# Kernel tuning notes

Hardware: AMD Instinct MI355X
Metric: run time of the kernel (lower is better)

Reference implementation:

```python
import jax, jax.numpy as jnp
import numpy as np

HEADS = 8
LN_EPS = 1e-5


def _layernorm(x, g, b):
    mu = x.mean(-1, keepdims=True)
    var = jnp.var(x, axis=-1, keepdims=True)  # biased, matches torch LayerNorm
    return (x - mu) / jnp.sqrt(var + LN_EPS) * g + b


def setup_inputs() -> dict:
    key = jax.random.key(0)
    ks = jax.random.split(key, 5)
    Q, N, D = 4, 2048, 512  # [query-groups, tokens, model dim]
    return {
        "q": jax.random.normal(ks[0], (Q, N, D), jnp.float32),
        "k": jax.random.normal(ks[1], (Q, N, D), jnp.float32),
        "v": jax.random.normal(ks[2], (Q, N, D), jnp.float32),
        "ln_gamma": jnp.ones((D,), jnp.float32),
        "ln_beta": jnp.zeros((D,), jnp.float32),
        "w_in": jax.random.normal(ks[3], (D, D), jnp.float32) * 0.02,   # torch Linear weight [inner_dim, dim]
        "w_out": jax.random.normal(ks[4], (D, D), jnp.float32) * 0.02,  # [dim, inner_dim]
        "b_out": jnp.zeros((D,), jnp.float32),
        "cov_w_raw": jnp.float32(0.6),
        "var_w_raw": jnp.float32(0.2),
    }


def reference(q, k, v, ln_gamma, ln_beta, w_in, w_out, b_out, cov_w_raw, var_w_raw):
    H = HEADS

    def proj(t):
        x = _layernorm(t, ln_gamma, ln_beta) @ w_in.T  # [Q,N,inner]
        Qd, Nd, I = x.shape
        return x.reshape(Qd, Nd, H, I // H).transpose(2, 0, 1, 3)  # [H,Q,N,d]

    f_q, f_k, f_v = proj(q), proj(k), proj(v)
    d = f_q.shape[-1]

    # cosine similarity component
    dots = jnp.einsum('hqnd,hqmd->hqnm', f_q, f_k)
    qn = jnp.linalg.norm(f_q, axis=-1)  # [H,Q,N]
    kn = jnp.linalg.norm(f_k, axis=-1)
    cosine_sim = dots / (qn[..., :, None] * kn[..., None, :])

    # centered covariance component
    qc = f_q - f_q.mean(-1, keepdims=True)
    kc = f_k - f_k.mean(-1, keepdims=True)
    cov_component = jnp.einsum('hqnd,hqmd->hqnm', qc, kc) / d

    # variance product component (torch.var is unbiased -> ddof=1)
    q_var = jnp.var(f_q, axis=-1, ddof=1)  # [H,Q,N]
    k_var = jnp.var(f_k, axis=-1, ddof=1)
    var_component = q_var[..., :, None] * k_var[..., None, :] / d

    cov_w = jax.nn.sigmoid(cov_w_raw)
    var_w = jax.nn.sigmoid(var_w_raw)
    cos_w = 1.0 - cov_w - var_w
    attn = cos_w * cosine_sim + cov_w * cov_component + var_w * var_component

    out = jnp.einsum('hqnm,hqmd->hqnd', attn, f_v)
    out = out.transpose(1, 2, 0, 3).reshape(q.shape[0], q.shape[1], -1)  # q n (h d)
    return out @ w_out.T + b_out
```

## Files before the change

kernel.cpp:

```cpp
#include <hip/hip_runtime.h>
#include <hip/hip_bf16.h>
#include <math.h>

#define D_MODEL 512
#define NTOK 2048
#define QGRP 4
#define NHEAD 8
#define HDIM 64
#define ROWS_PER_T (QGRP * NTOK)
#define LN_EPS 1e-5f
#define NCHUNK 16

typedef __attribute__((ext_vector_type(8))) short short8;
typedef __attribute__((ext_vector_type(8))) __bf16 bf16x8;
typedef __attribute__((ext_vector_type(4))) float f32x4;

__device__ inline void split2(float y, ushort& h, ushort& l) {
    __hip_bfloat16 hb = __float2bfloat16(y);
    float hf = __bfloat162float(hb);
    __hip_bfloat16 lb = __float2bfloat16(y - hf);
    h = *reinterpret_cast<ushort*>(&hb);
    l = *reinterpret_cast<ushort*>(&lb);
}

__device__ inline float b2f(ushort u) {
    unsigned int x = ((unsigned int)u) << 16;
    return __uint_as_float(x);
}

__device__ inline void split8v(const float4& p0, const float4& p1, bf16x8& bh, bf16x8& bl) {
    float xv[8] = {p0.x, p0.y, p0.z, p0.w, p1.x, p1.y, p1.z, p1.w};
    ushort hs[8], ls[8];
#pragma unroll
    for (int j = 0; j < 8; ++j) split2(xv[j], hs[j], ls[j]);
    bh = *(const bf16x8*)hs;
    bl = *(const bf16x8*)ls;
}

__global__ __launch_bounds__(256)
void ln_split3_kernel(const float* __restrict__ q, const float* __restrict__ k,
                      const float* __restrict__ v, const float* __restrict__ gamma,
                      const float* __restrict__ beta,
                      ushort* __restrict__ A3h, ushort* __restrict__ A3l) {
    int wave = threadIdx.x >> 6, lane = threadIdx.x & 63;
    size_t row = (size_t)blockIdx.x * 4 + wave;
    int t = (int)(row >> 13);
    size_t r = row & 8191;
    const float* src = (t == 0 ? q : (t == 1 ? k : v)) + r * D_MODEL + lane * 8;
    float4 a = *(const float4*)src;
    float4 b = *(const float4*)(src + 4);
    float s  = a.x + a.y + a.z + a.w + b.x + b.y + b.z + b.w;
    float sq = a.x*a.x + a.y*a.y + a.z*a.z + a.w*a.w
             + b.x*b.x + b.y*b.y + b.z*b.z + b.w*b.w;
    for (int m = 1; m < 64; m <<= 1) {
        s  += __shfl_xor(s, m);
        sq += __shfl_xor(sq, m);
    }
    float mu   = s * (1.0f / (float)D_MODEL);
    float var  = sq * (1.0f / (float)D_MODEL) - mu * mu;
    float rstd = 1.0f / sqrtf(var + LN_EPS);
    float4 g0 = *(const float4*)(gamma + lane * 8);
    float4 g1 = *(const float4*)(gamma + lane * 8 + 4);
    float4 t0 = *(const float4*)(beta + lane * 8);
    float4 t1 = *(const float4*)(beta + lane * 8 + 4);
    float xv[8] = {a.x, a.y, a.z, a.w, b.x, b.y, b.z, b.w};
    float gv[8] = {g0.x, g0.y, g0.z, g0.w, g1.x, g1.y, g1.z, g1.w};
    float bv[8] = {t0.x, t0.y, t0.z, t0.w, t1.x, t1.y, t1.z, t1.w};
    ushort hs[8], ls[8];
#pragma unroll
    for (int j = 0; j < 8; ++j) {
        float y = (xv[j] - mu) * rstd * gv[j] + bv[j];
        split2(y, hs[j], ls[j]);
    }
    *(short8*)(A3h + row * D_MODEL + lane * 8) = *(const short8*)hs;
    *(short8*)(A3l + row * D_MODEL + lane * 8) = *(const short8*)ls;
}

__global__ __launch_bounds__(256)
void split_mat2_kernel(const float* __restrict__ W0, const float* __restrict__ W1,
                       ushort* __restrict__ Wh0, ushort* __restrict__ Wl0,
                       ushort* __restrict__ Wh1, ushort* __restrict__ Wl1) {
    int half = blockIdx.x >> 7;
    const float* W = half ? W1 : W0;
    ushort* Wh = half ? Wh1 : Wh0;
    ushort* Wl = half ? Wl1 : Wl0;
    size_t i = ((size_t)(blockIdx.x & 127) * 256 + threadIdx.x) * 8;
    float4 a = *(const float4*)(W + i);
    float4 b = *(const float4*)(W + i + 4);
    float xv[8] = {a.x, a.y, a.z, a.w, b.x, b.y, b.z, b.w};
    ushort hs[8], ls[8];
#pragma unroll
    for (int j = 0; j < 8; ++j) split2(xv[j], hs[j], ls[j]);
    *(short8*)(Wh + i) = *(const short8*)hs;
    *(short8*)(Wl + i) = *(const short8*)ls;
}

template <int MODE>
__global__ __launch_bounds__(256)
void gemm_split_kernel(const ushort* __restrict__ Ah, const ushort* __restrict__ Al,
                       const ushort* __restrict__ Wh, const ushort* __restrict__ Wl,
                       const float* __restrict__ bias, float* __restrict__ C,
                       ushort* __restrict__ Ch, ushort* __restrict__ Cl) {
    __shared__ __align__(16) ushort sA[2][128][32];
    __shared__ __align__(16) ushort sW[2][128][32];
    int tid  = threadIdx.x;
    int lane = tid & 63, wid = tid >> 6;
    int wr = wid >> 1, wc = wid & 1;
    int z, xblk;
    if (MODE == 3) { z = blockIdx.x % 3; xblk = blockIdx.x / 3; }
    else           { z = 0;              xblk = blockIdx.x;     }
    size_t rowBase = (size_t)xblk * 128;
    size_t colBase = (size_t)blockIdx.y * 128;
    size_t zoff = (size_t)z * ROWS_PER_T * D_MODEL;
    const ushort* gA[2] = {Ah + zoff, Al + zoff};
    const ushort* gW[2] = {Wh, Wl};

    int sr = tid >> 2;
    int sc8 = tid & 3;

    short8 st[8];

#define LOADK(KT)                                                                  \
    {                                                                              \
        int idx = 0;                                                               \
        _Pragma("unroll")                                                          \
        for (int hl = 0; hl < 2; ++hl)                                             \
            _Pragma("unroll")                                                      \
            for (int p = 0; p < 2; ++p) {                                          \
                int r = p * 64 + sr;                                               \
                st[idx++] = *(const short8*)(gA[hl] + (rowBase + r) * D_MODEL +    \
                                             (KT) + sc8 * 8);                      \
            }                                                                      \
        _Pragma("unroll")                                                          \
        for (int hl = 0; hl < 2; ++hl)                                             \
            _Pragma("unroll")                                                      \
            for (int p = 0; p < 2; ++p) {                                          \
                int r = p * 64 + sr;                                               \
                st[idx++] = *(const short8*)(gW[hl] + (colBase + r) * D_MODEL +    \
                                             (KT) + sc8 * 8);                      \
            }                                                                      \
    }

    f32x4 acc[4][4] = {};

    LOADK(0);
    for (int step = 0; step < 16; ++step) {
        __syncthreads();
        {
            int idx = 0;
#pragma unroll
            for (int hl = 0; hl < 2; ++hl)
#pragma unroll
                for (int p = 0; p < 2; ++p) {
                    int r = p * 64 + sr;
                    *(short8*)&sA[hl][r][(sc8 ^ ((r >> 1) & 3)) << 3] = st[idx++];
                }
#pragma unroll
            for (int hl = 0; hl < 2; ++hl)
#pragma unroll
                for (int p = 0; p < 2; ++p) {
                    int r = p * 64 + sr;
                    *(short8*)&sW[hl][r][(sc8 ^ ((r >> 1) & 3)) << 3] = st[idx++];
                }
        }
        __syncthreads();
        if (step < 15) LOADK((step + 1) * 32);
        {
            bf16x8 aH[4], aL[4];
#pragma unroll
            for (int m = 0; m < 4; ++m) {
                int r = wr * 64 + m * 16 + (lane & 15);
                int cs = ((lane >> 4) ^ ((r >> 1) & 3)) << 3;
                aH[m] = *(const bf16x8*)&sA[0][r][cs];
                aL[m] = *(const bf16x8*)&sA[1][r][cs];
            }
#pragma unroll
            for (int n = 0; n < 4; ++n) {
                int rc = wc * 64 + n * 16 + (lane & 15);
                int cs = ((lane >> 4) ^ ((rc >> 1) & 3)) << 3;
                bf16x8 bH = *(const bf16x8*)&sW[0][rc][cs];
                bf16x8 bL = *(const bf16x8*)&sW[1][rc][cs];
#pragma unroll
                for (int m = 0; m < 4; ++m) {
                    acc[m][n] = __builtin_amdgcn_mfma_f32_16x16x32_bf16(aL[m], bH, acc[m][n], 0, 0, 0);
                    acc[m][n] = __builtin_amdgcn_mfma_f32_16x16x32_bf16(aH[m], bL, acc[m][n], 0, 0, 0);
                    acc[m][n] = __builtin_amdgcn_mfma_f32_16x16x32_bf16(aH[m], bH, acc[m][n], 0, 0, 0);
                }
            }
        }
    }
#pragma unroll
    for (int m = 0; m < 4; ++m)
#pragma unroll
        for (int n = 0; n < 4; ++n) {
            size_t col = colBase + wc * 64 + n * 16 + (lane & 15);
            size_t rb  = rowBase + wr * 64 + m * 16 + ((lane >> 4) << 2);
            if (MODE == 3) {
                if (z == 0) {
#pragma unroll
                    for (int r = 0; r < 4; ++r) {
                        ushort oh, ol;
                        split2(acc[m][n][r], oh, ol);
                        Ch[(rb + r) * D_MODEL + col] = oh;
                        Cl[(rb + r) * D_MODEL + col] = ol;
                    }
                } else {
                    float* Cz = C + (size_t)(z - 1) * ROWS_PER_T * D_MODEL;
#pragma unroll
                    for (int r = 0; r < 4; ++r)
                        Cz[(rb + r) * D_MODEL + col] = acc[m][n][r];
                }
            } else {
                float bv = bias[col];
#pragma unroll
                for (int r = 0; r < 4; ++r)
                    C[(rb + r) * D_MODEL + col] = acc[m][n][r] + bv;
            }
        }
#undef LOADK
}

__global__ __launch_bounds__(256)
void pair_reduce_mfma_kernel(const float* __restrict__ fk, const float* __restrict__ fv,
                             float* __restrict__ partials) {
    int pc = blockIdx.x;
    int pair = pc >> 4, chunk = pc & 15;
    int h = pair & 7, qg = pair >> 3;
    const float* Fk = fk + ((size_t)(qg * NTOK + chunk * 128)) * D_MODEL + h * HDIM;
    const float* Fv = fv + ((size_t)(qg * NTOK + chunk * 128)) * D_MODEL + h * HDIM;
    __shared__ float fkT[64][132];
    __shared__ float fvT[64][132];
    __shared__ float rkn_s[128], kvar_s[128];
    __shared__ float uvp[4][64];
    int tid = threadIdx.x, lane = tid & 63, wid = tid >> 6;
    int tn = tid >> 2;
    int fb = (tid & 3) << 2;
#pragma unroll
    for (int pass = 0; pass < 2; ++pass) {
        int n = pass * 64 + tn;
        float x[16], y[16];
#pragma unroll
        for (int j4 = 0; j4 < 4; ++j4) {
            *(float4*)&x[j4 * 4] = *(const float4*)(Fk + (size_t)n * D_MODEL + fb + j4 * 16);
            *(float4*)&y[j4 * 4] = *(const float4*)(Fv + (size_t)n * D_MODEL + fb + j4 * 16);
        }
        float s = 0.f, sq = 0.f;
#pragma unroll
        for (int j = 0; j < 16; ++j) { s += x[j]; sq += x[j] * x[j]; }
        s  += __shfl_xor(s, 1);  s  += __shfl_xor(s, 2);
        sq += __shfl_xor(sq, 1); sq += __shfl_xor(sq, 2);
        if ((tid & 3) == 0) {
            rkn_s[n]  = 1.0f / sqrtf(sq);
            kvar_s[n] = (sq - s * s * (1.0f / 64.0f)) * (1.0f / 63.0f);
        }
#pragma unroll
        for (int j4 = 0; j4 < 4; ++j4)
#pragma unroll
            for (int i = 0; i < 4; ++i) {
                fkT[fb + j4 * 16 + i][n] = x[j4 * 4 + i];
                fvT[fb + j4 * 16 + i][n] = y[j4 * 4 + i];
            }
    }
    __syncthreads();

    {
        float acc = 0.f;
#pragma unroll
        for (int j4 = 0; j4 < 8; ++j4) {
            float4 kv  = *(const float4*)&kvar_s[wid * 32 + j4 * 4];
            float4 f4  = *(const float4*)&fvT[lane][wid * 32 + j4 * 4];
            acc += kv.x * f4.x + kv.y * f4.y + kv.z * f4.z + kv.w * f4.w;
        }
        uvp[wid][lane] = acc;
    }

    int wm = wid >> 1, wn = wid & 1;
    int fr = lane & 15, kg = (lane >> 4) << 3;
    f32x4 accP[2][2] = {}, accC[2][2] = {};
#pragma unroll
    for (int t = 0; t < 4; ++t) {
        int k0 = t * 32 + kg;
        float4 rk0 = *(const float4*)&rkn_s[k0];
        float4 rk1 = *(const float4*)&rkn_s[k0 + 4];
        bf16x8 aRH[2], aRL[2], aSH[2], aSL[2], bH[2], bL[2];
#pragma unroll
        for (int m = 0; m < 2; ++m) {
            int a = wm * 32 + m * 16 + fr;
            float4 r0 = *(const float4*)&fkT[a][k0];
            float4 r1 = *(const float4*)&fkT[a][k0 + 4];
            split8v(r0, r1, aRH[m], aRL[m]);
            float4 s0 = make_float4(r0.x * rk0.x, r0.y * rk0.y, r0.z * rk0.z, r0.w * rk0.w);
            float4 s1 = make_float4(r1.x * rk1.x, r1.y * rk1.y, r1.z * rk1.z, r1.w * rk1.w);
            split8v(s0, s1, aSH[m], aSL[m]);
        }
#pragma unroll
        for (int n = 0; n < 2; ++n) {
            int c = wn * 32 + n * 16 + fr;
            float4 r0 = *(const float4*)&fvT[c][k0];
            float4 r1 = *(const float4*)&fvT[c][k0 + 4];
            split8v(r0, r1, bH[n], bL[n]);
        }
#pragma unroll
        for (int m = 0; m < 2; ++m)
#pragma unroll
            for (int n = 0; n < 2; ++n) {
                accP[m][n] = __builtin_amdgcn_mfma_f32_16x16x32_bf16(aSL[m], bH[n], accP[m][n], 0, 0, 0);
                accP[m][n] = __builtin_amdgcn_mfma_f32_16x16x32_bf16(aSH[m], bL[n], accP[m][n], 0, 0, 0);
                accP[m][n] = __builtin_amdgcn_mfma_f32_16x16x32_bf16(aSH[m], bH[n], accP[m][n], 0, 0, 0);
                accC[m][n] = __builtin_amdgcn_mfma_f32_16x16x32_bf16(aRL[m], bH[n], accC[m][n], 0, 0, 0);
                accC[m][n] = __builtin_amdgcn_mfma_f32_16x16x32_bf16(aRH[m], bL[n], accC[m][n], 0, 0, 0);
                accC[m][n] = __builtin_amdgcn_mfma_f32_16x16x32_bf16(aRH[m], bH[n], accC[m][n], 0, 0, 0);
            }
    }

    float* outp = partials + (size_t)pc * 8256;
#pragma unroll
    for (int m = 0; m < 2; ++m)
#pragma unroll
        for (int n = 0; n < 2; ++n) {
            int a0 = wm * 32 + m * 16 + ((lane >> 4) << 2);
            int c  = wn * 32 + n * 16 + fr;
#pragma unroll
            for (int r = 0; r < 4; ++r) {
                outp[(a0 + r) * 64 + c]        = accP[m][n][r];
                outp[4096 + (a0 + r) * 64 + c] = accC[m][n][r];
            }
        }
    __syncthreads();
    if (tid < 64)
        outp[8192 + tid] = uvp[0][tid] + uvp[1][tid] + uvp[2][tid] + uvp[3][tid];
}

__global__ __launch_bounds__(256)
void pair_finalize_kernel(const float* __restrict__ partials, float* __restrict__ pairacc) {
    int pair = blockIdx.x >> 3, sl = blockIdx.x & 7;
    int e0 = sl * 1032, e1 = e0 + 1032;
    for (int e = e0 + threadIdx.x; e < e1; e += 256) {
        float s = 0.f;
        for (int c = 0; c < NCHUNK; ++c)
            s += partials[((size_t)(pair * NCHUNK + c)) * 8256 + e];
        pairacc[(size_t)pair * 8320 + e] = s;
    }
}

__global__ __launch_bounds__(256)
void q_apply_mfma_kernel(const ushort* __restrict__ Fqh, const ushort* __restrict__ Fql,
                         const float* __restrict__ pairacc,
                         const float* __restrict__ cov_raw, const float* __restrict__ var_raw,
                         ushort* __restrict__ Oh, ushort* __restrict__ Ol) {
    int pair = blockIdx.x >> 4, chunk = blockIdx.x & 15;
    int h = pair & 7, qg = pair >> 3;
    __shared__ float PT[64][68];
    __shared__ float CT[64][68];
    __shared__ float u_s[64], sc_s[64];
    const float* pa = pairacc + (size_t)pair * 8320;
    for (int e = threadIdx.x; e < 4096; e += 256) {
        int a = e >> 6, c = e & 63;
        PT[c][a] = pa[e];
        CT[c][a] = pa[4096 + e];
    }
    if (threadIdx.x < 64) u_s[threadIdx.x] = pa[8192 + threadIdx.x];
    __syncthreads();
    if (threadIdx.x < 64) {
        float s = 0.f;
#pragma unroll
        for (int a = 0; a < 64; ++a) s += CT[threadIdx.x][a];
        sc_s[threadIdx.x] = s;
    }
    __syncthreads();
    int tid = threadIdx.x, lane = tid & 63, wave = tid >> 6;
    size_t row0 = (size_t)qg * NTOK + (size_t)chunk * 128 + wave * 32;
    const ushort* qhp = Fqh + row0 * D_MODEL + h * HDIM;
    const ushort* qlp = Fql + row0 * D_MODEL + h * HDIM;

    bf16x8 aH[2][2], aL[2][2];
    float qsum[2], qsq[2];
#pragma unroll
    for (int m = 0; m < 2; ++m) {
        int r = m * 16 + (lane & 15);
        int k0 = (lane >> 4) * 8;
        float s = 0.f, sq = 0.f;
#pragma unroll
        for (int ks = 0; ks < 2; ++ks) {
            short8 hv = *(const short8*)(qhp + (size_t)r * D_MODEL + ks * 32 + k0);
            short8 lv = *(const short8*)(qlp + (size_t)r * D_MODEL + ks * 32 + k0);
            aH[m][ks] = *(const bf16x8*)&hv;
            aL[m][ks] = *(const bf16x8*)&lv;
#pragma unroll
            for (int j = 0; j < 8; ++j) {
                float val = b2f((ushort)hv[j]) + b2f((ushort)lv[j]);
                s += val; sq += val * val;
            }
        }
        s  += __shfl_xor(s, 16);  s  += __shfl_xor(s, 32);
        sq += __shfl_xor(sq, 16); sq += __shfl_xor(sq, 32);
        qsum[m] = s; qsq[m] = sq;
    }

    f32x4 accP[2][4] = {}, accC[2][4] = {};
#pragma unroll
    for (int n = 0; n < 4; ++n) {
        int c = n * 16 + (lane & 15);
#pragma unroll
        for (int ks = 0; ks < 2; ++ks) {
            int kb = ks * 32 + (lane >> 4) * 8;
            {
                float4 p0 = *(const float4*)&PT[c][kb];
                float4 p1 = *(const float4*)&PT[c][kb + 4];
                bf16x8 bH, bL;
                split8v(p0, p1, bH, bL);
#pragma unroll
                for (int m = 0; m < 2; ++m) {
                    accP[m][n] = __builtin_amdgcn_mfma_f32_16x16x32_bf16(aL[m][ks], bH, accP[m][n], 0, 0, 0);
                    accP[m][n] = __builtin_amdgcn_mfma_f32_16x16x32_bf16(aH[m][ks], bL, accP[m][n], 0, 0, 0);
                    accP[m][n] = __builtin_amdgcn_mfma_f32_16x16x32_bf16(aH[m][ks], bH, accP[m][n], 0, 0, 0);
                }
            }
            {
                float4 p0 = *(const float4*)&CT[c][kb];
                float4 p1 = *(const float4*)&CT[c][kb + 4];
                bf16x8 bH, bL;
                split8v(p0, p1, bH, bL);
#pragma unroll
                for (int m = 0; m < 2; ++m) {
                    accC[m][n] = __builtin_amdgcn_mfma_f32_16x16x32_bf16(aL[m][ks], bH, accC[m][n], 0, 0, 0);
                    accC[m][n] = __builtin_amdgcn_mfma_f32_16x16x32_bf16(aH[m][ks], bL, accC[m][n], 0, 0, 0);
                    accC[m][n] = __builtin_amdgcn_mfma_f32_16x16x32_bf16(aH[m][ks], bH, accC[m][n], 0, 0, 0);
                }
            }
        }
    }

    float cw = 1.0f / (1.0f + expf(-cov_raw[0]));
    float vw = 1.0f / (1.0f + expf(-var_raw[0]));
    float cos_w = 1.0f - cw - vw;
    float cw_cov = cw * (1.0f / 64.0f);
    float cw_var = vw * (1.0f / 64.0f);
#pragma unroll
    for (int n = 0; n < 4; ++n) {
        int c = n * 16 + (lane & 15);
        float u_c  = u_s[c];
        float sc_c = sc_s[c];
#pragma unroll
        for (int m = 0; m < 2; ++m)
#pragma unroll
            for (int i = 0; i < 4; ++i) {
                int rp = ((lane >> 4) << 2) + i;
                float s  = __shfl(qsum[m], rp);
                float sq = __shfl(qsq[m], rp);
                float qmean = s * (1.0f / 64.0f);
                float rqn   = 1.0f / sqrtf(sq);
                float qvar  = (sq - s * qmean) * (1.0f / 63.0f);
                float res = cos_w * rqn * accP[m][n][i]
                          + cw_cov * (accC[m][n][i] - qmean * sc_c)
                          + cw_var * qvar * u_c;
                ushort oh, ol;
                split2(res, oh, ol);
                size_t o = (row0 + m * 16 + rp) * D_MODEL + h * HDIM + c;
                Oh[o] = oh;
                Ol[o] = ol;
            }
    }
}

extern "C" void kernel_launch(void* const* d_in, const int* in_sizes, int n_in,
                              void* d_out, int out_size, void* d_ws, size_t ws_size,
                              hipStream_t stream) {
    const float* q     = (const float*)d_in[0];
    const float* k     = (const float*)d_in[1];
    const float* v     = (const float*)d_in[2];
    const float* gamma = (const float*)d_in[3];
    const float* beta  = (const float*)d_in[4];
    const float* w_in  = (const float*)d_in[5];
    const float* w_out = (const float*)d_in[6];
    const float* b_out = (const float*)d_in[7];
    const float* cov_r = (const float*)d_in[8];
    const float* var_r = (const float*)d_in[9];
    float* out = (float*)d_out;

    const size_t E = (size_t)ROWS_PER_T * D_MODEL;
    float*  ws       = (float*)d_ws;
    float*  fk       = ws;
    float*  fv       = fk + E;
    ushort* Fqh      = (ushort*)(fv + E);
    ushort* Fql      = Fqh + E;
    ushort* A3h      = Fql + E;
    ushort* A3l      = A3h + 3 * E;
    ushort* Whi      = A3l + 3 * E;
    ushort* Wli      = Whi + D_MODEL * D_MODEL;
    ushort* Who      = Wli + D_MODEL * D_MODEL;
    ushort* Wlo      = Who + D_MODEL * D_MODEL;
    ushort* Oh       = Wlo + D_MODEL * D_MODEL;
    ushort* Ol       = Oh + E;
    float*  partials = (float*)(Ol + E);
    float*  pairacc  = partials + (size_t)32 * NCHUNK * 8256;

    hipLaunchKernelGGL(split_mat2_kernel, dim3(256), dim3(256), 0, stream,
                       w_in, w_out, Whi, Wli, Who, Wlo);
    hipLaunchKernelGGL(ln_split3_kernel, dim3(3 * ROWS_PER_T / 4), dim3(256), 0, stream,
                       q, k, v, gamma, beta, A3h, A3l);
    hipLaunchKernelGGL((gemm_split_kernel<3>), dim3(192, 4), dim3(256), 0, stream,
                       A3h, A3l, Whi, Wli, (const float*)nullptr, fk, Fqh, Fql);
    hipLaunchKernelGGL(pair_reduce_mfma_kernel, dim3(32 * NCHUNK), dim3(256), 0, stream,
                       fk, fv, partials);
    hipLaunchKernelGGL(pair_finalize_kernel, dim3(32 * 8), dim3(256), 0, stream,
                       partials, pairacc);
    hipLaunchKernelGGL(q_apply_mfma_kernel, dim3(512), dim3(256), 0, stream,
                       Fqh, Fql, pairacc, cov_r, var_r, Oh, Ol);
    hipLaunchKernelGGL((gemm_split_kernel<2>), dim3(ROWS_PER_T / 128, 4), dim3(256), 0, stream,
                       Oh, Ol, Who, Wlo, b_out, out, (ushort*)nullptr, (ushort*)nullptr);
}
```

Baseline: 125.2 us.

## Use direct global-to-LDS loads in split GEMM and merge prep kernels

The GEMM now loads its tiles with global_load_lds, which writes global data straight into shared memory. Each wave fills one of the four tile buffers, and the XOR swizzle is moved to the global source address. This replaces the register-staged prefetch with a synchronous issue between barriers, so the load overlap from the old software pipeline is lost. Separately, the weight-split kernel is folded into the layernorm-split kernel as extra blocks, which saves one launch.

```diff
diff --git a/kernel.cpp b/kernel.cpp
--- a/kernel.cpp
+++ b/kernel.cpp
@@ -37,11 +37,37 @@
     bl = *(const bf16x8*)ls;
 }
 
+__device__ inline void gload16(const void* g, void* l) {
+    __builtin_amdgcn_global_load_lds(
+        (const __attribute__((address_space(1))) void*)g,
+        (__attribute__((address_space(3))) void*)l, 16, 0, 0);
+}
+
 __global__ __launch_bounds__(256)
-void ln_split3_kernel(const float* __restrict__ q, const float* __restrict__ k,
-                      const float* __restrict__ v, const float* __restrict__ gamma,
-                      const float* __restrict__ beta,
-                      ushort* __restrict__ A3h, ushort* __restrict__ A3l) {
+void prep_kernel(const float* __restrict__ q, const float* __restrict__ k,
+                 const float* __restrict__ v, const float* __restrict__ gamma,
+                 const float* __restrict__ beta,
+                 const float* __restrict__ W0, const float* __restrict__ W1,
+                 ushort* __restrict__ A3h, ushort* __restrict__ A3l,
+                 ushort* __restrict__ Wh0, ushort* __restrict__ Wl0,
+                 ushort* __restrict__ Wh1, ushort* __restrict__ Wl1) {
+    if (blockIdx.x >= 6144) {
+        int b = blockIdx.x - 6144;
+        int half = b >> 7;
+        const float* W = half ? W1 : W0;
+        ushort* Wh = half ? Wh1 : Wh0;
+        ushort* Wl = half ? Wl1 : Wl0;
+        size_t i = ((size_t)(b & 127) * 256 + threadIdx.x) * 8;
+        float4 a = *(const float4*)(W + i);
+        float4 bb = *(const float4*)(W + i + 4);
+        float xv[8] = {a.x, a.y, a.z, a.w, bb.x, bb.y, bb.z, bb.w};
+        ushort hs[8], ls[8];
+#pragma unroll
+        for (int j = 0; j < 8; ++j) split2(xv[j], hs[j], ls[j]);
+        *(short8*)(Wh + i) = *(const short8*)hs;
+        *(short8*)(Wl + i) = *(const short8*)ls;
+        return;
+    }
     int wave = threadIdx.x >> 6, lane = threadIdx.x & 63;
     size_t row = (size_t)blockIdx.x * 4 + wave;
     int t = (int)(row >> 13);
@@ -74,25 +100,6 @@
     }
     *(short8*)(A3h + row * D_MODEL + lane * 8) = *(const short8*)hs;
     *(short8*)(A3l + row * D_MODEL + lane * 8) = *(const short8*)ls;
-}
-
-__global__ __launch_bounds__(256)
-void split_mat2_kernel(const float* __restrict__ W0, const float* __restrict__ W1,
-                       ushort* __restrict__ Wh0, ushort* __restrict__ Wl0,
-                       ushort* __restrict__ Wh1, ushort* __restrict__ Wl1) {
-    int half = blockIdx.x >> 7;
-    const float* W = half ? W1 : W0;
-    ushort* Wh = half ? Wh1 : Wh0;
-    ushort* Wl = half ? Wl1 : Wl0;
-    size_t i = ((size_t)(blockIdx.x & 127) * 256 + threadIdx.x) * 8;
-    float4 a = *(const float4*)(W + i);
-    float4 b = *(const float4*)(W + i + 4);
-    float xv[8] = {a.x, a.y, a.z, a.w, b.x, b.y, b.z, b.w};
-    ushort hs[8], ls[8];
-#pragma unroll
-    for (int j = 0; j < 8; ++j) split2(xv[j], hs[j], ls[j]);
-    *(short8*)(Wh + i) = *(const short8*)hs;
-    *(short8*)(Wl + i) = *(const short8*)ls;
 }
 
 template <int MODE>
@@ -115,56 +122,30 @@
     const ushort* gA[2] = {Ah + zoff, Al + zoff};
     const ushort* gW[2] = {Wh, Wl};
 
-    int sr = tid >> 2;
-    int sc8 = tid & 3;
-
-    short8 st[8];
-
-#define LOADK(KT)                                                                  \
-    {                                                                              \
-        int idx = 0;                                                               \
-        _Pragma("unroll")                                                          \
-        for (int hl = 0; hl < 2; ++hl)                                             \
-            _Pragma("unroll")                                                      \
-            for (int p = 0; p < 2; ++p) {                                          \
-                int r = p * 64 + sr;                                               \
-                st[idx++] = *(const short8*)(gA[hl] + (rowBase + r) * D_MODEL +    \
-                                             (KT) + sc8 * 8);                      \
-            }                                                                      \
-        _Pragma("unroll")                                                          \
-        for (int hl = 0; hl < 2; ++hl)                                             \
-            _Pragma("unroll")                                                      \
-            for (int p = 0; p < 2; ++p) {                                          \
-                int r = p * 64 + sr;                                               \
-                st[idx++] = *(const short8*)(gW[hl] + (colBase + r) * D_MODEL +    \
-                                             (KT) + sc8 * 8);                      \
-            }                                                                      \
+    const ushort* gsrc;
+    ushort* ldsTile;
+    {
+        int rIC = lane >> 2;
+        int gsw = (((lane & 3) ^ ((lane >> 3) & 3)) << 3);
+        if (wid == 0)      { gsrc = gA[0] + (rowBase + rIC) * D_MODEL + gsw; ldsTile = &sA[0][0][0]; }
+        else if (wid == 1) { gsrc = gA[1] + (rowBase + rIC) * D_MODEL + gsw; ldsTile = &sA[1][0][0]; }
+        else if (wid == 2) { gsrc = gW[0] + (colBase + rIC) * D_MODEL + gsw; ldsTile = &sW[0][0][0]; }
+        else               { gsrc = gW[1] + (colBase + rIC) * D_MODEL + gsw; ldsTile = &sW[1][0][0]; }
+    }
+
+#define ISSUE(KT)                                                              \
+    {                                                                          \
+        _Pragma("unroll")                                                      \
+        for (int j = 0; j < 8; ++j)                                            \
+            gload16(gsrc + (size_t)j * 16 * D_MODEL + (KT), ldsTile + j * 512);\
     }
 
     f32x4 acc[4][4] = {};
 
-    LOADK(0);
     for (int step = 0; step < 16; ++step) {
         __syncthreads();
-        {
-            int idx = 0;
-#pragma unroll
-            for (int hl = 0; hl < 2; ++hl)
-#pragma unroll
-                for (int p = 0; p < 2; ++p) {
-                    int r = p * 64 + sr;
-                    *(short8*)&sA[hl][r][(sc8 ^ ((r >> 1) & 3)) << 3] = st[idx++];
-                }
-#pragma unroll
-            for (int hl = 0; hl < 2; ++hl)
-#pragma unroll
-                for (int p = 0; p < 2; ++p) {
-                    int r = p * 64 + sr;
-                    *(short8*)&sW[hl][r][(sc8 ^ ((r >> 1) & 3)) << 3] = st[idx++];
-                }
-        }
+        ISSUE(step * 32);
         __syncthreads();
-        if (step < 15) LOADK((step + 1) * 32);
         {
             bf16x8 aH[4], aL[4];
 #pragma unroll
@@ -217,7 +198,7 @@
                     C[(rb + r) * D_MODEL + col] = acc[m][n][r] + bv;
             }
         }
-#undef LOADK
+#undef ISSUE
 }
 
 __global__ __launch_bounds__(256)
@@ -495,10 +476,9 @@
     float*  partials = (float*)(Ol + E);
     float*  pairacc  = partials + (size_t)32 * NCHUNK * 8256;
 
-    hipLaunchKernelGGL(split_mat2_kernel, dim3(256), dim3(256), 0, stream,
-                       w_in, w_out, Whi, Wli, Who, Wlo);
-    hipLaunchKernelGGL(ln_split3_kernel, dim3(3 * ROWS_PER_T / 4), dim3(256), 0, stream,
-                       q, k, v, gamma, beta, A3h, A3l);
+    hipLaunchKernelGGL(prep_kernel, dim3(3 * ROWS_PER_T / 4 + 256), dim3(256), 0, stream,
+                       q, k, v, gamma, beta, w_in, w_out,
+                       A3h, A3l, Whi, Wli, Who, Wlo);
     hipLaunchKernelGGL((gemm_split_kernel<3>), dim3(192, 4), dim3(256), 0, stream,
                        A3h, A3l, Whi, Wli, (const float*)nullptr, fk, Fqh, Fql);
     hipLaunchKernelGGL(pair_reduce_mfma_kernel, dim3(32 * NCHUNK), dim3(256), 0, stream,
```

After: 131.0 us. +4.6%, slower.
